# Performance work log

Hardware: AMD Instinct MI355X
Metric: run time of the kernel (lower is better)

Reference implementation:

```python
import jax, jax.numpy as jnp
import numpy as np

# NOTE: SoftAttn (not shown in source) is assumed to be a channel-wise softmax over the
# kernel_size**2 attention maps, as is standard in involution/dynamic-conv designs.

def conv2d(x, w, b=None, stride=1, pad=0, dil=1):
    y = jax.lax.conv_general_dilated(
        x, w, (stride, stride), [(pad, pad), (pad, pad)],
        rhs_dilation=(dil, dil), dimension_numbers=('NCHW', 'OIHW', 'NCHW'))
    return y if b is None else y + b[None, :, None, None]

def prelu(x, a):
    return jnp.where(x >= 0, x, a * x)

def pixel_shuffle(x, r):
    b, c, h, w = x.shape
    x = x.reshape(b, c // (r * r), r, r, h, w)
    x = x.transpose(0, 1, 4, 2, 5, 3)  # b, c', h, r, w, r
    return x.reshape(b, c // (r * r), h * r, w * r)

def aflb(x, aw, ab, fw):
    # Adaptive Fine-grained Local Block: per-position attention over k^2 taps,
    # broadcast across input channels, then contracted with the conv weight.
    k = 3
    C = x.shape[1]
    att = jax.nn.softmax(conv2d(x, aw, ab, pad=1), axis=1)  # [b, k*k, H, W]
    # unfold (channel-major, spatial-minor, matching torch F.unfold)
    p = jax.lax.conv_general_dilated_patches(
        x, (k, k), (1, 1), [(1, 1), (1, 1)],
        dimension_numbers=('NCHW', 'OIHW', 'NCHW'))  # [b, C*k*k, H, W]
    b_, _, H, W = p.shape
    p = p.reshape(b_, C, k * k, H, W)
    atx = p * att[:, None]  # broadcast attention over channels
    return jnp.einsum('bcphw,ocp->bohw', atx, fw.reshape(fw.shape[0], C, k * k))

def rmrs(x, wa, ba, wb, bb, wc, bc, awA, abA, fwA, awB, abB, fwB):
    o = jnp.concatenate([
        conv2d(x, wa, ba, pad=1),
        conv2d(x, wb, bb, pad=2, dil=2),
        conv2d(x, wc, bc, pad=3, dil=3)], axis=1)
    o = aflb(o, awA, abA, fwA)
    o = aflb(o, awB, abB, fwB)
    return jax.nn.relu(o + x)


def setup_inputs() -> dict:
    key = jax.random.key(0)
    ks = iter(jax.random.split(key, 64))
    def rn(shape, s=0.05):
        return jax.random.normal(next(ks), shape, jnp.float32) * s
    a = lambda: jnp.full((1,), 0.25, jnp.float32)
    d = dict(
        ms_up=rn((2, 4, 256, 256), 1.0),
        ms_org=rn((2, 4, 64, 64), 1.0),
        pan=rn((2, 1, 256, 256), 1.0),
        w_up4=rn((64, 4, 3, 3)), b_up4=jnp.zeros(64, jnp.float32), a_up4=a(),
        w_blk53=rn((30, 5, 3, 3)), b_blk53=jnp.zeros(30, jnp.float32), a_blk53=a(),
        w_blk43=rn((30, 4, 3, 3)), b_blk43=jnp.zeros(30, jnp.float32), a_blk43=a(),
        w1a=rn((20, 60, 3, 3)), b1a=jnp.zeros(20, jnp.float32),
        w1b=rn((20, 60, 3, 3)), b1b=jnp.zeros(20, jnp.float32),
        w1c=rn((20, 60, 3, 3)), b1c=jnp.zeros(20, jnp.float32),
        aw1=rn((9, 60, 3, 3)), ab1=jnp.zeros(9, jnp.float32), fw1=rn((60, 60, 3, 3)),
        aw2=rn((9, 60, 3, 3)), ab2=jnp.zeros(9, jnp.float32), fw2=rn((60, 60, 3, 3)),
        w_blk2=rn((30, 60, 3, 3)), b_blk2=jnp.zeros(30, jnp.float32), a_blk2=a(),
        w2a=rn((10, 30, 3, 3)), b2a=jnp.zeros(10, jnp.float32),
        w2b=rn((10, 30, 3, 3)), b2b=jnp.zeros(10, jnp.float32),
        w2c=rn((10, 30, 3, 3)), b2c=jnp.zeros(10, jnp.float32),
        aw3=rn((9, 30, 3, 3)), ab3=jnp.zeros(9, jnp.float32), fw3=rn((30, 30, 3, 3)),
        aw4=rn((9, 30, 3, 3)), ab4=jnp.zeros(9, jnp.float32), fw4=rn((30, 30, 3, 3)),
        w_c6=rn((4, 30, 3, 3)), b_c6=jnp.zeros(4, jnp.float32),
    )
    return d


def reference(ms_up, ms_org, pan,
              w_up4, b_up4, a_up4,
              w_blk53, b_blk53, a_blk53,
              w_blk43, b_blk43, a_blk43,
              w1a, b1a, w1b, b1b, w1c, b1c,
              aw1, ab1, fw1, aw2, ab2, fw2,
              w_blk2, b_blk2, a_blk2,
              w2a, b2a, w2b, b2b, w2c, b2c,
              aw3, ab3, fw3, aw4, ab4, fw4,
              w_c6, b_c6):
    ms_org_up = prelu(pixel_shuffle(conv2d(ms_org, w_up4, b_up4, pad=1), 4), a_up4)
    data1 = jnp.concatenate([ms_org_up, pan], axis=1)  # [b,5,H,W]
    pan_conv = prelu(conv2d(data1, w_blk53, b_blk53, pad=1), a_blk53)
    ms_up_conv = prelu(conv2d(ms_up, w_blk43, b_blk43, pad=1), a_blk43)
    out1 = jnp.concatenate([ms_up_conv, pan_conv], axis=1)  # [b,60,H,W]
    out2 = rmrs(out1, w1a, b1a, w1b, b1b, w1c, b1c, aw1, ab1, fw1, aw2, ab2, fw2)
    out3 = prelu(conv2d(out2, w_blk2, b_blk2, pad=1), a_blk2)  # [b,30,H,W]
    out3 = rmrs(out3, w2a, b2a, w2b, b2b, w2c, b2c, aw3, ab3, fw3, aw4, ab4, fw4)
    out8 = conv2d(out3, w_c6, b_c6, pad=1)
    return out8 + ms_up
```

## Files before the change

### kernel.cpp

```cpp
#include <hip/hip_runtime.h>

typedef __attribute__((ext_vector_type(8))) short short8;
typedef __attribute__((ext_vector_type(4))) float f32x4;
typedef __attribute__((ext_vector_type(4))) int i32x4;

#define HW 65536

__device__ __forceinline__ float bf2f(unsigned short u){
    union { unsigned int i; float f; } x; x.i = ((unsigned int)u) << 16; return x.f;
}
__device__ __forceinline__ unsigned short f2bf(float f){
    union { float f; unsigned int i; } x; x.f = f;
    unsigned int r = x.i + 0x7fffu + ((x.i >> 16) & 1u);
    return (unsigned short)(r >> 16);
}
__device__ __forceinline__ unsigned int pack2(float a, float b){
    return (unsigned int)f2bf(a) | ((unsigned int)f2bf(b) << 16);
}
__device__ __forceinline__ i32x4 addrelu4(i32x4 a, i32x4 b){
    i32x4 o;
#pragma unroll
    for (int k = 0; k < 4; ++k) {
        unsigned int ua = (unsigned int)a[k], ub = (unsigned int)b[k];
        float x0 = bf2f((unsigned short)(ua & 0xffff)) + bf2f((unsigned short)(ub & 0xffff));
        float x1 = bf2f((unsigned short)(ua >> 16))    + bf2f((unsigned short)(ub >> 16));
        o[k] = (int)(((unsigned int)f2bf(fmaxf(x0, 0.f))) |
                     ((unsigned int)f2bf(fmaxf(x1, 0.f)) << 16));
    }
    return o;
}

template<int KK, int PRELU>
__global__ __launch_bounds__(256, 4) void sconv_k(
    const unsigned short* __restrict__ in,
    const unsigned short* __restrict__ wfrag,
    const float* __restrict__ bias,
    const float* __restrict__ alphap,
    unsigned short* __restrict__ outb, int cpad, int coff)
{
    constexpr int CPIN = KK * 32, SGR = KK * 4, SGRP = SGR + 1, SPX = 66;
    constexpr int NSTGDW = 3 * SPX * SGRP * 4;
    constexpr int ODP = 20;
    constexpr int OUTOFF = NSTGDW;
    __shared__ __align__(16) unsigned int sm[NSTGDW + 64 * ODP];
    const int tid = threadIdx.x;
    const int lane = tid & 63, wv = tid >> 6;
    const int col = lane & 15, g = lane >> 4;
    const int bx = blockIdx.x;
    const int xcd = bx & 7, t = bx >> 3;
    const int y0 = xcd * 32 + (t & 31);
    const int x0 = ((t >> 5) & 3) * 64;
    const int b = blockIdx.z;
    const unsigned short* inb = in + (size_t)b * HW * CPIN;

#pragma unroll
    for (int rr = 0; rr < 3; ++rr) {
        const int yy = y0 + rr - 1;
        for (int u = tid; u < SPX * SGR; u += 256) {
            const int slot = u & (SGR - 1), px = u / SGR;
            const int xx = x0 - 1 + px;
            i32x4 v = {0,0,0,0};
            if ((unsigned)yy < 256u && (unsigned)xx < 256u)
                v = *(const i32x4*)(inb + (size_t)(yy * 256 + xx) * CPIN + slot * 8);
            *(i32x4*)&sm[((rr * SPX + px) * SGRP + slot) * 4] = v;
        }
    }
    if (tid < 64) sm[OUTOFF + tid * ODP + 15] = 0;
    __syncthreads();

    const short8* wp = (const short8*)wfrag;
    f32x4 acc[2][2];
#pragma unroll
    for (int mt = 0; mt < 2; ++mt)
#pragma unroll
        for (int c = 0; c < 2; ++c) acc[mt][c] = (f32x4){0.f,0.f,0.f,0.f};
#pragma unroll
    for (int tap = 0; tap < 9; ++tap) {
        const int dy = tap / 3 - 1, dx = tap % 3 - 1;
        const int rl = dy + 1;
        short8 af[2][KK];
#pragma unroll
        for (int mt = 0; mt < 2; ++mt)
#pragma unroll
            for (int kk = 0; kk < KK; ++kk)
                af[mt][kk] = wp[((tap * 2 + mt) * KK + kk) * 64 + lane];
        const int pl = 1 + wv * 16 + col + dx;
#pragma unroll
        for (int kk = 0; kk < KK; ++kk) {
            const int c2 = (KK == 2) ? kk : (tap & 1);
            short8 bf = *(const short8*)&sm[((rl * SPX + pl) * SGRP + kk * 4 + g) * 4];
#pragma unroll
            for (int mt = 0; mt < 2; ++mt)
                acc[mt][c2] = __builtin_amdgcn_mfma_f32_16x16x32_bf16(af[mt][kk], bf, acc[mt][c2], 0, 0, 0);
        }
    }
    const float al = PRELU ? __ldg(alphap) : 0.f;
    const int px = wv * 16 + col;
#pragma unroll
    for (int mt = 0; mt < 2; ++mt) {
        const f32x4 a = acc[mt][0] + acc[mt][1];
#pragma unroll
        for (int e = 0; e < 2; ++e) {
            const int rb = mt * 16 + g * 4 + e * 2;
            if (rb < 30) {
                float v0 = a[e * 2]     + __ldg(bias + rb);
                float v1 = a[e * 2 + 1] + ((rb + 1 < 30) ? __ldg(bias + rb + 1) : 0.f);
                if (PRELU) { v0 = v0 >= 0.f ? v0 : al * v0; v1 = v1 >= 0.f ? v1 : al * v1; }
                if (rb + 1 >= 30) v1 = 0.f;
                sm[OUTOFF + px * ODP + (rb >> 1)] = pack2(v0, v1);
            }
        }
    }
    __syncthreads();
    {
        const int slot = tid & 3, opx = tid >> 2;
        i32x4 v = *(i32x4*)&sm[OUTOFF + opx * ODP + slot * 4];
        const size_t go = ((size_t)b * HW + (size_t)y0 * 256 + x0 + opx) * cpad + coff + slot * 8;
        *(i32x4*)(outb + go) = v;
    }
}

template<int KK, int MR>
__global__ __launch_bounds__(256, 4) void trident_s(
    const unsigned short* __restrict__ in,
    const unsigned short* __restrict__ wf0, const unsigned short* __restrict__ wf1,
    const unsigned short* __restrict__ wf2,
    const float* __restrict__ b0, const float* __restrict__ b1, const float* __restrict__ b2,
    unsigned short* __restrict__ outb)
{
    constexpr int CPIN = KK * 32, CPAD = KK * 32;
    constexpr int SGR = KK * 4, SGRP = SGR + 1, SPX = 70;
    constexpr int MT_ = (KK == 2) ? 2 : 1;
    constexpr int CPP = KK * 4, ODP = (CPP + 1) * 4;
    constexpr int NSTGDW = 3 * SPX * SGRP * 4;
    constexpr int OUTOFF = NSTGDW;
    constexpr int NG1 = SPX * SGR;
    constexpr int NIT2 = (2 * NG1 + 255) / 256;
    __shared__ __align__(16) unsigned int sm[NSTGDW + 64 * ODP];
    const int tid = threadIdx.x;
    const int lane = tid & 63, wv = tid >> 6;
    const int col = lane & 15, g = lane >> 4;
    const int bx = blockIdx.x;
    const int xcd = bx & 7, t = bx >> 3;
    const int y0 = xcd * 32 + (t & 31);
    const int x0 = ((t >> 5) & 3) * 64;
    const int b = blockIdx.z;
    const unsigned short* inb = in + (size_t)b * HW * CPIN;

    auto stage_row = [&](int srow, int yy) {
        for (int u = tid; u < NG1; u += 256) {
            const int slot = u & (SGR - 1), px = u / SGR;
            const int xx = x0 - 3 + px;
            i32x4 v = {0,0,0,0};
            if ((unsigned)yy < 256u && (unsigned)xx < 256u)
                v = *(const i32x4*)(inb + (size_t)(yy * 256 + xx) * CPIN + slot * 8);
            *(i32x4*)&sm[((srow * SPX + px) * SGRP + slot) * 4] = v;
        }
    };
    i32x4 Rp[NIT2];
    auto issue_pair = [&](int d) {
#pragma unroll
        for (int it = 0; it < NIT2; ++it) {
            const int u = tid + it * 256;
            i32x4 v = {0,0,0,0};
            if (u < 2 * NG1) {
                const int r = (u >= NG1) ? 1 : 0;
                const int uu = u - r * NG1;
                const int slot = uu & (SGR - 1), px = uu / SGR;
                const int yy = y0 + (r ? d : -d);
                const int xx = x0 - 3 + px;
                if ((unsigned)yy < 256u && (unsigned)xx < 256u)
                    v = *(const i32x4*)(inb + (size_t)(yy * 256 + xx) * CPIN + slot * 8);
            }
            Rp[it] = v;
        }
    };
    auto write_pair = [&]() {
#pragma unroll
        for (int it = 0; it < NIT2; ++it) {
            const int u = tid + it * 256;
            if (u < 2 * NG1) {
                const int r = (u >= NG1) ? 1 : 0;
                const int uu = u - r * NG1;
                const int slot = uu & (SGR - 1), px = uu / SGR;
                *(i32x4*)&sm[(((1 + r) * SPX + px) * SGRP + slot) * 4] = Rp[it];
            }
        }
    };
    auto do_conv = [&](int d, const unsigned short* wfx, const float* bs, int which) {
        const short8* wp = (const short8*)wfx;
        f32x4 acc[MT_][2];
#pragma unroll
        for (int mt = 0; mt < MT_; ++mt)
#pragma unroll
            for (int c = 0; c < 2; ++c) acc[mt][c] = (f32x4){0.f,0.f,0.f,0.f};
#pragma unroll
        for (int tap = 0; tap < 9; ++tap) {
            const int dy = tap / 3 - 1, dx = tap % 3 - 1;
            const int rl = (dy == 0) ? 0 : (dy < 0 ? 1 : 2);
            short8 af[MT_][KK];
#pragma unroll
            for (int mt = 0; mt < MT_; ++mt)
#pragma unroll
                for (int kk = 0; kk < KK; ++kk)
                    af[mt][kk] = wp[((tap * MT_ + mt) * KK + kk) * 64 + lane];
            const int pl = 3 + wv * 16 + col + dx * d;
#pragma unroll
            for (int kk = 0; kk < KK; ++kk) {
                const int c2 = (KK == 2) ? kk : (tap & 1);
                short8 bf = *(const short8*)&sm[((rl * SPX + pl) * SGRP + kk * 4 + g) * 4];
#pragma unroll
                for (int mt = 0; mt < MT_; ++mt)
                    acc[mt][c2] = __builtin_amdgcn_mfma_f32_16x16x32_bf16(af[mt][kk], bf, acc[mt][c2], 0, 0, 0);
            }
        }
        const int px = wv * 16 + col;
#pragma unroll
        for (int mt = 0; mt < MT_; ++mt) {
            const f32x4 a = acc[mt][0] + acc[mt][1];
#pragma unroll
            for (int e = 0; e < 2; ++e) {
                const int rb = mt * 16 + g * 4 + e * 2;
                if (rb < MR) {
                    float v0 = a[e * 2]     + __ldg(bs + rb);
                    float v1 = a[e * 2 + 1] + ((rb + 1 < MR) ? __ldg(bs + rb + 1) : 0.f);
                    if (rb + 1 >= MR) v1 = 0.f;
                    sm[OUTOFF + px * ODP + ((which * MR + rb) >> 1)] = pack2(v0, v1);
                }
            }
        }
    };

    stage_row(0, y0); stage_row(1, y0 - 1); stage_row(2, y0 + 1);
    issue_pair(2);
    if (tid < 64) {
#pragma unroll
        for (int dwp = 3 * MR / 2; dwp < CPP * 4; ++dwp) sm[OUTOFF + tid * ODP + dwp] = 0;
    }
    __syncthreads();

    do_conv(1, wf0, b0, 0);
    __syncthreads();
    write_pair();
    issue_pair(3);
    __syncthreads();

    do_conv(2, wf1, b1, 1);
    __syncthreads();
    write_pair();
    __syncthreads();

    do_conv(3, wf2, b2, 2);
    __syncthreads();

    for (int u = tid; u < 64 * CPP; u += 256) {
        const int slot = u & (CPP - 1), opx = u / CPP;
        i32x4 v = *(i32x4*)&sm[OUTOFF + opx * ODP + slot * 4];
        const size_t go = ((size_t)b * HW + (size_t)y0 * 256 + x0 + opx) * CPAD + slot * 8;
        *(i32x4*)(outb + go) = v;
    }
}

template<int KK, int RPB, int RES>
__global__ __launch_bounds__(256, 4) void aflb_p(
    const unsigned short* __restrict__ in,
    const unsigned short* __restrict__ awf, const float* __restrict__ ab,
    const unsigned short* __restrict__ fwf,
    const unsigned short* __restrict__ res,
    unsigned short* __restrict__ outb)
{
    constexpr int CPIN = KK * 32, MTT = 2 * KK, CPAD = 16 * MTT;
    constexpr int SROWS = RPB + 2, SPX = 66, SGR = KK * 4, SGRP = SGR + 1;
    constexpr int CPP = CPAD / 8, ODP = (CPP + 1) * 4;
    constexpr int NSTGDW = SROWS * SPX * SGRP * 4;
    constexpr int ATOFF = NSTGDW;
    constexpr int NATT = RPB * 64 * 9;
    constexpr int OUTOFF = ATOFF + NATT;
    __shared__ __align__(16) unsigned int sm[OUTOFF + RPB * 64 * ODP];

    const int tid = threadIdx.x;
    const int lane = tid & 63, wv = tid >> 6;
    const int col = lane & 15, g = lane >> 4;
    const int bx = blockIdx.x;
    const int xcd = bx & 7, t = bx >> 3;
    const int y0 = (RPB == 1) ? (xcd * 32 + (t & 31)) : (xcd * 32 + (t & 15) * 2);
    const int xseg = (RPB == 1) ? ((t >> 5) & 3) : ((t >> 4) & 3);
    const int x0 = xseg * 64;
    const int b = blockIdx.z;
    const unsigned short* inb = in + (size_t)b * HW * CPIN;

    for (int u = tid; u < SROWS * SPX * SGR; u += 256) {
        const int slot = u & (SGR - 1);
        const int px = (u / SGR) % SPX;
        const int row = u / (SGR * SPX);
        const int yy = y0 + row - 1, xx = x0 - 1 + px;
        i32x4 v = {0,0,0,0};
        if ((unsigned)yy < 256u && (unsigned)xx < 256u)
            v = *(const i32x4*)(inb + (size_t)(yy * 256 + xx) * CPIN + slot * 8);
        *(i32x4*)&sm[((row * SPX + px) * SGRP + slot) * 4] = v;
    }
    __syncthreads();

    const short8* awp = (const short8*)awf;
    const short8* fwp = (const short8*)fwf;

    constexpr int NF1 = (RPB == 1) ? 1 : 2;
    const int arow = (RPB == 1) ? 0 : (wv >> 1);
    const int apx0 = (RPB == 1) ? (wv * 16) : ((wv & 1) * 32);
    f32x4 aacc[NF1][2];
#pragma unroll
    for (int nf = 0; nf < NF1; ++nf)
#pragma unroll
        for (int c = 0; c < 2; ++c) aacc[nf][c] = (f32x4){0.f,0.f,0.f,0.f};
#pragma unroll
    for (int tap = 0; tap < 9; ++tap) {
        const int dy = tap / 3 - 1, dx = tap % 3 - 1;
        const int rl = arow + dy + 1;
        short8 afa[KK];
#pragma unroll
        for (int kk = 0; kk < KK; ++kk)
            afa[kk] = awp[(tap * KK + kk) * 64 + lane];
#pragma unroll
        for (int nf = 0; nf < NF1; ++nf) {
            const int pl = 1 + apx0 + nf * 16 + col + dx;
#pragma unroll
            for (int kk = 0; kk < KK; ++kk) {
                const int c2 = (KK == 2) ? kk : (tap & 1);
                short8 bf = *(const short8*)&sm[((rl * SPX + pl) * SGRP + kk * 4 + g) * 4];
                aacc[nf][c2] = __builtin_amdgcn_mfma_f32_16x16x32_bf16(afa[kk], bf, aacc[nf][c2], 0, 0, 0);
            }
        }
    }
#pragma unroll
    for (int nf = 0; nf < NF1; ++nf) {
        const f32x4 aa = aacc[nf][0] + aacc[nf][1];
        float v[4];
        float m = -1e30f;
#pragma unroll
        for (int r = 0; r < 4; ++r) {
            const int row = g * 4 + r;
            v[r] = (row < 9) ? (aa[r] + __ldg(ab + row)) : -1e30f;
            m = fmaxf(m, v[r]);
        }
        m = fmaxf(m, __shfl_xor(m, 16));
        m = fmaxf(m, __shfl_xor(m, 32));
        float e[4]; float s = 0.f;
#pragma unroll
        for (int r = 0; r < 4; ++r) { e[r] = (g * 4 + r < 9) ? __expf(v[r] - m) : 0.f; s += e[r]; }
        s += __shfl_xor(s, 16);
        s += __shfl_xor(s, 32);
        const float inv = 1.f / s;
        const int px = apx0 + nf * 16 + col;
#pragma unroll
        for (int r = 0; r < 4; ++r) {
            const int row = g * 4 + r;
            if (row < 9) sm[ATOFF + (arow * 64 + px) * 9 + row] = __float_as_uint(e[r] * inv);
        }
    }
    __syncthreads();

    const int prow = (RPB == 1) ? 0 : (wv >> 1);
    const int mth  = (RPB == 1) ? (wv >> 1) : 0;
    const int nfh  = wv & 1;
    f32x4 acc[2][2];
#pragma unroll
    for (int mtl = 0; mtl < 2; ++mtl)
#pragma unroll
        for (int nf = 0; nf < 2; ++nf) acc[mtl][nf] = (f32x4){0.f,0.f,0.f,0.f};
#pragma unroll
    for (int tap = 0; tap < 9; ++tap) {
        const int dy = tap / 3 - 1, dx = tap % 3 - 1;
        const int rl = prow + dy + 1;
        float av[2];
#pragma unroll
        for (int nf = 0; nf < 2; ++nf)
            av[nf] = __uint_as_float(sm[ATOFF + (prow * 64 + nfh * 32 + nf * 16 + col) * 9 + tap]);
        short8 af[2][KK];
#pragma unroll
        for (int mtl = 0; mtl < 2; ++mtl)
#pragma unroll
            for (int kk = 0; kk < KK; ++kk)
                af[mtl][kk] = fwp[((tap * MTT + (RPB == 1 ? mth * 2 + mtl : mtl)) * KK + kk) * 64 + lane];
#pragma unroll
        for (int nf = 0; nf < 2; ++nf) {
            const int pl = 1 + nfh * 32 + nf * 16 + col + dx;
            f32x4 p[2];
            p[0] = (f32x4){0.f,0.f,0.f,0.f}; p[1] = (f32x4){0.f,0.f,0.f,0.f};
#pragma unroll
            for (int kk = 0; kk < KK; ++kk) {
                short8 bf = *(const short8*)&sm[((rl * SPX + pl) * SGRP + kk * 4 + g) * 4];
#pragma unroll
                for (int mtl = 0; mtl < 2; ++mtl)
                    p[mtl] = __builtin_amdgcn_mfma_f32_16x16x32_bf16(af[mtl][kk], bf, p[mtl], 0, 0, 0);
            }
#pragma unroll
            for (int mtl = 0; mtl < 2; ++mtl)
#pragma unroll
                for (int r = 0; r < 4; ++r)
                    acc[mtl][nf][r] = fmaf(av[nf], p[mtl][r], acc[mtl][nf][r]);
        }
    }
    __syncthreads();

#pragma unroll
    for (int mtl = 0; mtl < 2; ++mtl) {
        const int mt = (RPB == 1) ? (mth * 2 + mtl) : mtl;
#pragma unroll
        for (int nf = 0; nf < 2; ++nf) {
            const int px = nfh * 32 + nf * 16 + col;
            const int base = OUTOFF + ((RPB == 2 ? prow * 64 : 0) + px) * ODP;
            const int rp = mt * 8 + g * 2;
            unsigned long long w =
                (unsigned long long)pack2(acc[mtl][nf][0], acc[mtl][nf][1]) |
                ((unsigned long long)pack2(acc[mtl][nf][2], acc[mtl][nf][3]) << 32);
            *(unsigned long long*)&sm[base + rp] = w;
        }
    }
    __syncthreads();

    constexpr int NOUT = RPB * 64 * CPP;
    for (int u = tid; u < NOUT; u += 256) {
        const int slot = u & (CPP - 1);
        const int px = (u / CPP) & 63;
        const int r = (RPB == 2) ? (u / (CPP * 64)) : 0;
        i32x4 v = *(i32x4*)&sm[OUTOFF + ((r * 64 + px) * ODP) + slot * 4];
        const size_t go = ((size_t)b * HW + (size_t)(y0 + r) * 256 + x0 + px) * CPAD + slot * 8;
        if (RES) v = addrelu4(v, *(const i32x4*)(res + go));
        *(i32x4*)(outb + go) = v;
    }
}

__global__ __launch_bounds__(256, 4) void final_k(
    const unsigned short* __restrict__ in,
    const unsigned short* __restrict__ wfrag,
    const float* __restrict__ bias,
    const float* __restrict__ msup, float* __restrict__ outf)
{
    constexpr int CPIN = 32, NF = 2;
    const int lane = threadIdx.x & 63, wv = threadIdx.x >> 6;
    const int col = lane & 15, g = lane >> 4;
    const int bx = blockIdx.x;
    const int xcd = bx & 7, t = bx >> 3;
    const int y = xcd * 32 + (t & 31);
    const int xh = t >> 5;
    const int b = blockIdx.z;
    const int x0 = xh * 128 + wv * 32;

    const unsigned short* inb = in + (size_t)b * HW * CPIN;
    const short8 kz = {0,0,0,0,0,0,0,0};
    const short8* wp = (const short8*)wfrag;

    f32x4 acc[NF];
#pragma unroll
    for (int nf = 0; nf < NF; ++nf) acc[nf] = (f32x4){0.f,0.f,0.f,0.f};
#pragma unroll
    for (int tap = 0; tap < 9; ++tap) {
        const int dy = tap / 3 - 1, dx = tap % 3 - 1;
        const int yy = y + dy;
        const bool yok = (unsigned)yy < 256u;
        const short8 af = wp[tap * 64 + lane];
#pragma unroll
        for (int nf = 0; nf < NF; ++nf) {
            const int xx = x0 + nf * 16 + col + dx;
            const bool ok = yok && ((unsigned)xx < 256u);
            const int pix = ok ? (yy * 256 + xx) : 0;
            short8 bf = *(const short8*)(inb + (size_t)pix * CPIN + g * 8);
            if (!ok) bf = kz;
            acc[nf] = __builtin_amdgcn_mfma_f32_16x16x32_bf16(af, bf, acc[nf], 0, 0, 0);
        }
    }
#pragma unroll
    for (int nf = 0; nf < NF; ++nf) {
        const int pix = y * 256 + x0 + nf * 16 + col;
        if (g == 0) {
#pragma unroll
            for (int r = 0; r < 4; ++r) {
                const size_t oi = ((size_t)b * 4 + r) * HW + pix;
                outf[oi] = acc[nf][r] + __ldg(bias + r) + msup[oi];
            }
        }
    }
}

struct PrepDesc { const float* src; int cout, cin, kksh, mtsh, flags, dstoff, n; };
struct PrepArgs { PrepDesc d[18]; };

__global__ __launch_bounds__(256) void prep_k(PrepArgs pa, unsigned short* __restrict__ wb)
{
    const PrepDesc d = pa.d[blockIdx.y];
    const int e = blockIdx.x * 256 + threadIdx.x;
    if (e >= d.n) return;
    const int j = e & 7;
    const int lane = (e >> 3) & 63;
    const int i512 = e >> 9;
    const int kk = i512 & ((1 << d.kksh) - 1);
    const int mt = (i512 >> d.kksh) & ((1 << d.mtsh) - 1);
    const int tap = i512 >> (d.kksh + d.mtsh);
    const int rpos = mt * 16 + (lane & 15);
    const int kpos = kk * 32 + (lane >> 4) * 8 + j;
    int o = rpos, ic = kpos;
    bool ok = true;
    if (d.flags & 2) {
        if (rpos < 30) o = rpos;
        else if (rpos >= 32 && rpos < 62) o = rpos - 2;
        else ok = false;
    }
    if (d.flags & 1) {
        if (kpos < 30) ic = kpos;
        else if (kpos >= 32 && kpos < 62) ic = kpos - 2;
        else ok = false;
    }
    float v = 0.f;
    if (ok && o < d.cout && ic < d.cin) v = d.src[(o * d.cin + ic) * 9 + tap];
    wb[d.dstoff + e] = f2bf(v);
}

template<int CIN, int COUT, int OCB, int H, int W>
__launch_bounds__(256)
__global__ void upconv_k(const float* __restrict__ in, const float* __restrict__ wgt,
                         const float* __restrict__ bias, float* __restrict__ out)
{
    constexpr int HWp = H * W;
    constexpr int NOCB = COUT / OCB;
    const int tx = threadIdx.x;
    const int lx = tx & 63, ly = tx >> 6;
    const int gx = blockIdx.x * 64 + lx;
    const int gy = blockIdx.y * 4 + ly;
    const int b = blockIdx.z / NOCB;
    const int ocb = blockIdx.z % NOCB;
    const int pixp = gy * W + gx;
    const float* inb = in + (size_t)b * CIN * HWp;

    int off[9]; float mul[9];
#pragma unroll
    for (int dy = 0; dy < 3; ++dy)
#pragma unroll
        for (int dx = 0; dx < 3; ++dx) {
            int p = dy * 3 + dx;
            int yy = gy + dy - 1, xx = gx + dx - 1;
            bool okp = ((unsigned)yy < (unsigned)H) && ((unsigned)xx < (unsigned)W);
            off[p] = okp ? (yy * W + xx) : 0;
            mul[p] = okp ? 1.f : 0.f;
        }
    float acc[OCB];
#pragma unroll
    for (int o = 0; o < OCB; ++o) acc[o] = 0.f;
    const float* wbase = wgt + (size_t)(ocb * OCB) * CIN * 9;
#pragma unroll
    for (int ic = 0; ic < CIN; ++ic) {
        const float* ip = inb + (size_t)ic * HWp;
        float tv[9];
#pragma unroll
        for (int p = 0; p < 9; ++p) tv[p] = __ldg(ip + off[p]) * mul[p];
#pragma unroll
        for (int o = 0; o < OCB; ++o) {
            const float* wq = wbase + (size_t)(o * CIN + ic) * 9;
#pragma unroll
            for (int p = 0; p < 9; ++p) acc[o] = fmaf(tv[p], wq[p], acc[o]);
        }
    }
#pragma unroll
    for (int o = 0; o < OCB; ++o)
        out[((size_t)b * COUT + ocb * OCB + o) * HWp + pixp] = acc[o] + __ldg(bias + ocb * OCB + o);
}

__global__ __launch_bounds__(256) void build_inputs(
    const float* __restrict__ tup, const float* __restrict__ pan,
    const float* __restrict__ aup, const float* __restrict__ msup,
    unsigned short* __restrict__ data1, unsigned short* __restrict__ msb)
{
    const int i = blockIdx.x * 256 + threadIdx.x;
    const int b = i >> 16, pixp = i & 65535;
    const int y = pixp >> 8, x = pixp & 255;
    unsigned short o[32];
#pragma unroll
    for (int c = 0; c < 32; ++c) o[c] = 0;
    unsigned short* dst;
    if (blockIdx.y == 0) {
        const float a = __ldg(aup);
#pragma unroll
        for (int c = 0; c < 4; ++c) {
            const int ch = c * 16 + (y & 3) * 4 + (x & 3);
            float v = tup[(((size_t)b * 64 + ch) << 12) + ((y >> 2) << 6) + (x >> 2)];
            v = (v >= 0.f) ? v : a * v;
            o[c] = f2bf(v);
        }
        o[4] = f2bf(pan[((size_t)b << 16) + pixp]);
        dst = data1;
    } else {
#pragma unroll
        for (int c = 0; c < 4; ++c)
            o[c] = f2bf(msup[(((size_t)b * 4 + c) << 16) + pixp]);
        dst = msb;
    }
    short8* dp = (short8*)(dst + (size_t)i * 32);
#pragma unroll
    for (int q = 0; q < 4; ++q) {
        short8 s;
#pragma unroll
        for (int r = 0; r < 8; ++r) s[r] = (short)o[q * 8 + r];
        dp[q] = s;
    }
}

extern "C" void kernel_launch(void* const* d_in, const int* in_sizes, int n_in,
                              void* d_out, int out_size, void* d_ws, size_t ws_size,
                              hipStream_t stream) {
    const float* ms_up  = (const float*)d_in[0];
    const float* ms_org = (const float*)d_in[1];
    const float* pan    = (const float*)d_in[2];
    const float* w_up4  = (const float*)d_in[3];
    const float* b_up4  = (const float*)d_in[4];
    const float* a_up4  = (const float*)d_in[5];
    const float* w_blk53= (const float*)d_in[6];
    const float* b_blk53= (const float*)d_in[7];
    const float* a_blk53= (const float*)d_in[8];
    const float* w_blk43= (const float*)d_in[9];
    const float* b_blk43= (const float*)d_in[10];
    const float* a_blk43= (const float*)d_in[11];
    const float* w1a=(const float*)d_in[12]; const float* b1a=(const float*)d_in[13];
    const float* w1b=(const float*)d_in[14]; const float* b1b=(const float*)d_in[15];
    const float* w1c=(const float*)d_in[16]; const float* b1c=(const float*)d_in[17];
    const float* aw1=(const float*)d_in[18]; const float* ab1=(const float*)d_in[19];
    const float* fw1=(const float*)d_in[20];
    const float* aw2=(const float*)d_in[21]; const float* ab2=(const float*)d_in[22];
    const float* fw2=(const float*)d_in[23];
    const float* w_blk2=(const float*)d_in[24]; const float* b_blk2=(const float*)d_in[25]; const float* a_blk2=(const float*)d_in[26];
    const float* w2a=(const float*)d_in[27]; const float* b2a=(const float*)d_in[28];
    const float* w2b=(const float*)d_in[29]; const float* b2b=(const float*)d_in[30];
    const float* w2c=(const float*)d_in[31]; const float* b2c=(const float*)d_in[32];
    const float* aw3=(const float*)d_in[33]; const float* ab3=(const float*)d_in[34];
    const float* fw3=(const float*)d_in[35];
    const float* aw4=(const float*)d_in[36]; const float* ab4=(const float*)d_in[37];
    const float* fw4=(const float*)d_in[38];
    const float* w_c6=(const float*)d_in[39]; const float* b_c6=(const float*)d_in[40];

    float* out = (float*)d_out;
    char* ws = (char*)d_ws;

    const size_t BIG = (size_t)2 * HW * 64 * 2;
    const size_t HALF = BIG / 2;
    unsigned short* bufA = (unsigned short*)(ws);
    unsigned short* bufB = (unsigned short*)(ws + BIG);
    unsigned short* bufC = (unsigned short*)(ws + 2 * BIG);
    unsigned short* data1 = bufC;
    float*          t_up  = (float*)(ws + 2 * BIG + HALF);
    unsigned short* msb   = bufB;
    unsigned short* bufD = bufC;
    unsigned short* bufE = bufB;
    unsigned short* bufF = bufA;
    unsigned short* wb = (unsigned short*)(ws + 3 * BIG);

    if (ws_size < 3 * BIG + 1000000) return;

    PrepArgs pa;
    int off = 0, li = 0;
    auto add = [&](const float* s, int cout, int cin, int mtsh, int kksh, int flags) {
        const int n = 9 << (mtsh + kksh + 9);
        pa.d[li].src = s; pa.d[li].cout = cout; pa.d[li].cin = cin;
        pa.d[li].kksh = kksh; pa.d[li].mtsh = mtsh; pa.d[li].flags = flags;
        pa.d[li].dstoff = off; pa.d[li].n = n;
        int ret = off; off += n; ++li; return ret;
    };
    const int o_blk43 = add(w_blk43, 30, 4, 1, 0, 0);
    const int o_blk53 = add(w_blk53, 30, 5, 1, 0, 0);
    const int o_w1a   = add(w1a, 20, 60, 1, 1, 1);
    const int o_w1b   = add(w1b, 20, 60, 1, 1, 1);
    const int o_w1c   = add(w1c, 20, 60, 1, 1, 1);
    const int o_aw1   = add(aw1,  9, 60, 0, 1, 0);
    const int o_fw1   = add(fw1, 60, 60, 2, 1, 0);
    const int o_aw2   = add(aw2,  9, 60, 0, 1, 0);
    const int o_fw2   = add(fw2, 60, 60, 2, 1, 2);
    const int o_blk2  = add(w_blk2, 30, 60, 1, 1, 1);
    const int o_w2a   = add(w2a, 10, 30, 0, 0, 0);
    const int o_w2b   = add(w2b, 10, 30, 0, 0, 0);
    const int o_w2c   = add(w2c, 10, 30, 0, 0, 0);
    const int o_aw3   = add(aw3,  9, 30, 0, 0, 0);
    const int o_fw3   = add(fw3, 30, 30, 1, 0, 0);
    const int o_aw4   = add(aw4,  9, 30, 0, 0, 0);
    const int o_fw4   = add(fw4, 30, 30, 1, 0, 0);
    const int o_c6    = add(w_c6,  4, 30, 0, 0, 0);

    prep_k<<<dim3(144, 18), 256, 0, stream>>>(pa, wb);

    upconv_k<4, 64, 16, 64, 64><<<dim3(1, 16, 8), 256, 0, stream>>>(ms_org, w_up4, b_up4, t_up);
    build_inputs<<<dim3(512, 2), 256, 0, stream>>>(t_up, pan, a_up4, ms_up, data1, msb);

    const dim3 B256(256);
    const dim3 G1(1024, 1, 2);
    const dim3 GH(512, 1, 2);

    sconv_k<1,1><<<G1,B256,0,stream>>>(msb,   wb+o_blk43, b_blk43, a_blk43, bufA, 64, 0);
    sconv_k<1,1><<<G1,B256,0,stream>>>(data1, wb+o_blk53, b_blk53, a_blk53, bufA, 64, 32);

    trident_s<2,20><<<G1,B256,0,stream>>>(bufA, wb+o_w1a, wb+o_w1b, wb+o_w1c, b1a, b1b, b1c, bufB);
    aflb_p<2,1,0><<<G1,B256,0,stream>>>(bufB, wb+o_aw1, ab1, wb+o_fw1, nullptr, bufC);
    aflb_p<2,1,1><<<G1,B256,0,stream>>>(bufC, wb+o_aw2, ab2, wb+o_fw2, bufA,   bufB);

    sconv_k<2,1><<<G1,B256,0,stream>>>(bufB, wb+o_blk2, b_blk2, a_blk2, bufD, 32, 0);

    trident_s<1,10><<<G1,B256,0,stream>>>(bufD, wb+o_w2a, wb+o_w2b, wb+o_w2c, b2a, b2b, b2c, bufE);
    aflb_p<1,2,0><<<GH,B256,0,stream>>>(bufE, wb+o_aw3, ab3, wb+o_fw3, nullptr, bufF);
    aflb_p<1,2,1><<<GH,B256,0,stream>>>(bufF, wb+o_aw4, ab4, wb+o_fw4, bufD,   bufE);

    final_k<<<GH,B256,0,stream>>>(bufE, wb+o_c6, b_c6, ms_up, out);
}
```

Measured before the change: 205.8 us.

## Alias output staging onto input LDS buffer and raise occupancy launch bounds

Removes the separate output-staging region from shared memory in sconv, trident and aflb kernels by reusing the input staging area after a barrier. This shrinks the LDS footprint per block so more blocks can be resident, and the launch bounds are raised to request that higher occupancy. In trident, per-branch conv results are now held in registers until all three convs finish, which adds register pressure. The tighter launch bounds also risk register spills.

```diff
diff --git a/kernel.cpp b/kernel.cpp
--- a/kernel.cpp
+++ b/kernel.cpp
@@ -31,7 +31,7 @@
 }
 
 template<int KK, int PRELU>
-__global__ __launch_bounds__(256, 4) void sconv_k(
+__global__ __launch_bounds__(256, (KK == 2 ? 5 : 8)) void sconv_k(
     const unsigned short* __restrict__ in,
     const unsigned short* __restrict__ wfrag,
     const float* __restrict__ bias,
@@ -41,8 +41,7 @@
     constexpr int CPIN = KK * 32, SGR = KK * 4, SGRP = SGR + 1, SPX = 66;
     constexpr int NSTGDW = 3 * SPX * SGRP * 4;
     constexpr int ODP = 20;
-    constexpr int OUTOFF = NSTGDW;
-    __shared__ __align__(16) unsigned int sm[NSTGDW + 64 * ODP];
+    __shared__ __align__(16) unsigned int sm[NSTGDW];
     const int tid = threadIdx.x;
     const int lane = tid & 63, wv = tid >> 6;
     const int col = lane & 15, g = lane >> 4;
@@ -65,7 +64,6 @@
             *(i32x4*)&sm[((rr * SPX + px) * SGRP + slot) * 4] = v;
         }
     }
-    if (tid < 64) sm[OUTOFF + tid * ODP + 15] = 0;
     __syncthreads();
 
     const short8* wp = (const short8*)wfrag;
@@ -94,6 +92,8 @@
                 acc[mt][c2] = __builtin_amdgcn_mfma_f32_16x16x32_bf16(af[mt][kk], bf, acc[mt][c2], 0, 0, 0);
         }
     }
+    __syncthreads();
+
     const float al = PRELU ? __ldg(alphap) : 0.f;
     const int px = wv * 16 + col;
 #pragma unroll
@@ -102,26 +102,23 @@
 #pragma unroll
         for (int e = 0; e < 2; ++e) {
             const int rb = mt * 16 + g * 4 + e * 2;
-            if (rb < 30) {
-                float v0 = a[e * 2]     + __ldg(bias + rb);
-                float v1 = a[e * 2 + 1] + ((rb + 1 < 30) ? __ldg(bias + rb + 1) : 0.f);
-                if (PRELU) { v0 = v0 >= 0.f ? v0 : al * v0; v1 = v1 >= 0.f ? v1 : al * v1; }
-                if (rb + 1 >= 30) v1 = 0.f;
-                sm[OUTOFF + px * ODP + (rb >> 1)] = pack2(v0, v1);
-            }
+            float v0 = (rb < 30)     ? a[e * 2]     + __ldg(bias + rb)     : 0.f;
+            float v1 = (rb + 1 < 30) ? a[e * 2 + 1] + __ldg(bias + rb + 1) : 0.f;
+            if (PRELU) { v0 = v0 >= 0.f ? v0 : al * v0; v1 = v1 >= 0.f ? v1 : al * v1; }
+            sm[px * ODP + (rb >> 1)] = pack2(v0, v1);
         }
     }
     __syncthreads();
     {
         const int slot = tid & 3, opx = tid >> 2;
-        i32x4 v = *(i32x4*)&sm[OUTOFF + opx * ODP + slot * 4];
+        i32x4 v = *(i32x4*)&sm[opx * ODP + slot * 4];
         const size_t go = ((size_t)b * HW + (size_t)y0 * 256 + x0 + opx) * cpad + coff + slot * 8;
         *(i32x4*)(outb + go) = v;
     }
 }
 
 template<int KK, int MR>
-__global__ __launch_bounds__(256, 4) void trident_s(
+__global__ __launch_bounds__(256, (KK == 2 ? 5 : 8)) void trident_s(
     const unsigned short* __restrict__ in,
     const unsigned short* __restrict__ wf0, const unsigned short* __restrict__ wf1,
     const unsigned short* __restrict__ wf2,
@@ -133,10 +130,9 @@
     constexpr int MT_ = (KK == 2) ? 2 : 1;
     constexpr int CPP = KK * 4, ODP = (CPP + 1) * 4;
     constexpr int NSTGDW = 3 * SPX * SGRP * 4;
-    constexpr int OUTOFF = NSTGDW;
     constexpr int NG1 = SPX * SGR;
     constexpr int NIT2 = (2 * NG1 + 255) / 256;
-    __shared__ __align__(16) unsigned int sm[NSTGDW + 64 * ODP];
+    __shared__ __align__(16) unsigned int sm[NSTGDW];
     const int tid = threadIdx.x;
     const int lane = tid & 63, wv = tid >> 6;
     const int col = lane & 15, g = lane >> 4;
@@ -187,7 +183,9 @@
             }
         }
     };
-    auto do_conv = [&](int d, const unsigned short* wfx, const float* bs, int which) {
+
+    f32x4 resv[3][MT_];
+    auto do_conv = [&](int d, const unsigned short* wfx, int which) {
         const short8* wp = (const short8*)wfx;
         f32x4 acc[MT_][2];
 #pragma unroll
@@ -214,55 +212,62 @@
                     acc[mt][c2] = __builtin_amdgcn_mfma_f32_16x16x32_bf16(af[mt][kk], bf, acc[mt][c2], 0, 0, 0);
             }
         }
-        const int px = wv * 16 + col;
-#pragma unroll
-        for (int mt = 0; mt < MT_; ++mt) {
-            const f32x4 a = acc[mt][0] + acc[mt][1];
-#pragma unroll
-            for (int e = 0; e < 2; ++e) {
-                const int rb = mt * 16 + g * 4 + e * 2;
-                if (rb < MR) {
-                    float v0 = a[e * 2]     + __ldg(bs + rb);
-                    float v1 = a[e * 2 + 1] + ((rb + 1 < MR) ? __ldg(bs + rb + 1) : 0.f);
-                    if (rb + 1 >= MR) v1 = 0.f;
-                    sm[OUTOFF + px * ODP + ((which * MR + rb) >> 1)] = pack2(v0, v1);
-                }
-            }
-        }
+#pragma unroll
+        for (int mt = 0; mt < MT_; ++mt)
+            resv[which][mt] = acc[mt][0] + acc[mt][1];
     };
 
     stage_row(0, y0); stage_row(1, y0 - 1); stage_row(2, y0 + 1);
     issue_pair(2);
-    if (tid < 64) {
-#pragma unroll
-        for (int dwp = 3 * MR / 2; dwp < CPP * 4; ++dwp) sm[OUTOFF + tid * ODP + dwp] = 0;
-    }
-    __syncthreads();
-
-    do_conv(1, wf0, b0, 0);
+    __syncthreads();
+
+    do_conv(1, wf0, 0);
     __syncthreads();
     write_pair();
     issue_pair(3);
     __syncthreads();
 
-    do_conv(2, wf1, b1, 1);
+    do_conv(2, wf1, 1);
     __syncthreads();
     write_pair();
     __syncthreads();
 
-    do_conv(3, wf2, b2, 2);
+    do_conv(3, wf2, 2);
+    __syncthreads();
+
+    {
+        const float* bss[3] = {b0, b1, b2};
+        const int px = wv * 16 + col;
+#pragma unroll
+        for (int which = 0; which < 3; ++which)
+#pragma unroll
+            for (int mt = 0; mt < MT_; ++mt)
+#pragma unroll
+                for (int e = 0; e < 2; ++e) {
+                    const int rb = mt * 16 + g * 4 + e * 2;
+                    if (rb < MR) {
+                        float v0 = resv[which][mt][e * 2] + __ldg(bss[which] + rb);
+                        float v1 = (rb + 1 < MR) ? resv[which][mt][e * 2 + 1] + __ldg(bss[which] + rb + 1) : 0.f;
+                        sm[px * ODP + ((which * MR + rb) >> 1)] = pack2(v0, v1);
+                    }
+                }
+        if (tid < 64) {
+#pragma unroll
+            for (int dwp = 3 * MR / 2; dwp < CPP * 4; ++dwp) sm[tid * ODP + dwp] = 0;
+        }
+    }
     __syncthreads();
 
     for (int u = tid; u < 64 * CPP; u += 256) {
         const int slot = u & (CPP - 1), opx = u / CPP;
-        i32x4 v = *(i32x4*)&sm[OUTOFF + opx * ODP + slot * 4];
+        i32x4 v = *(i32x4*)&sm[opx * ODP + slot * 4];
         const size_t go = ((size_t)b * HW + (size_t)y0 * 256 + x0 + opx) * CPAD + slot * 8;
         *(i32x4*)(outb + go) = v;
     }
 }
 
 template<int KK, int RPB, int RES>
-__global__ __launch_bounds__(256, 4) void aflb_p(
+__global__ __launch_bounds__(256, (KK == 2 ? 5 : 6)) void aflb_p(
     const unsigned short* __restrict__ in,
     const unsigned short* __restrict__ awf, const float* __restrict__ ab,
     const unsigned short* __restrict__ fwf,
@@ -275,8 +280,7 @@
     constexpr int NSTGDW = SROWS * SPX * SGRP * 4;
     constexpr int ATOFF = NSTGDW;
     constexpr int NATT = RPB * 64 * 9;
-    constexpr int OUTOFF = ATOFF + NATT;
-    __shared__ __align__(16) unsigned int sm[OUTOFF + RPB * 64 * ODP];
+    __shared__ __align__(16) unsigned int sm[ATOFF + NATT];
 
     const int tid = threadIdx.x;
     const int lane = tid & 63, wv = tid >> 6;
@@ -408,7 +412,7 @@
 #pragma unroll
         for (int nf = 0; nf < 2; ++nf) {
             const int px = nfh * 32 + nf * 16 + col;
-            const int base = OUTOFF + ((RPB == 2 ? prow * 64 : 0) + px) * ODP;
+            const int base = ((RPB == 2 ? prow * 64 : 0) + px) * ODP;
             const int rp = mt * 8 + g * 2;
             unsigned long long w =
                 (unsigned long long)pack2(acc[mtl][nf][0], acc[mtl][nf][1]) |
@@ -423,14 +427,14 @@
         const int slot = u & (CPP - 1);
         const int px = (u / CPP) & 63;
         const int r = (RPB == 2) ? (u / (CPP * 64)) : 0;
-        i32x4 v = *(i32x4*)&sm[OUTOFF + ((r * 64 + px) * ODP) + slot * 4];
+        i32x4 v = *(i32x4*)&sm[((r * 64 + px) * ODP) + slot * 4];
         const size_t go = ((size_t)b * HW + (size_t)(y0 + r) * 256 + x0 + px) * CPAD + slot * 8;
         if (RES) v = addrelu4(v, *(const i32x4*)(res + go));
         *(i32x4*)(outb + go) = v;
     }
 }
 
-__global__ __launch_bounds__(256, 4) void final_k(
+__global__ __launch_bounds__(256, 8) void final_k(
     const unsigned short* __restrict__ in,
     const unsigned short* __restrict__ wfrag,
     const float* __restrict__ bias,
```

Result: slower. 216.1 us (+5.0%).

## Run trident dilation branches in parallel warps with swizzled 7-row LDS tile

Applied to the files above, without the earlier changes.

Replaces the sequential three-dilation trident kernel with one where 6 wavefronts (2 per dilation) compute the three dilated convolutions concurrently over a 32-pixel-wide tile. The whole 7-row halo is staged once, with an XOR swizzle in place of padded LDS strides, so the per-dilation row-pair reloads and intermediate barriers go away. Block size grows to 384 and the grid doubles. In exchange, horizontal halo overhead per block is higher (38 staged columns for 32 outputs) and each block loads more rows.

```diff
diff --git a/kernel.cpp b/kernel.cpp
--- a/kernel.cpp
+++ b/kernel.cpp
@@ -121,7 +121,7 @@
 }
 
 template<int KK, int MR>
-__global__ __launch_bounds__(256, 4) void trident_s(
+__global__ __launch_bounds__(384, 6) void trident_v(
     const unsigned short* __restrict__ in,
     const unsigned short* __restrict__ wf0, const unsigned short* __restrict__ wf1,
     const unsigned short* __restrict__ wf2,
@@ -129,92 +129,69 @@
     unsigned short* __restrict__ outb)
 {
     constexpr int CPIN = KK * 32, CPAD = KK * 32;
-    constexpr int SGR = KK * 4, SGRP = SGR + 1, SPX = 70;
+    constexpr int SGR = KK * 4, SWM = SGR - 1, SPX = 38, SROWS = 7;
     constexpr int MT_ = (KK == 2) ? 2 : 1;
-    constexpr int CPP = KK * 4, ODP = (CPP + 1) * 4;
-    constexpr int NSTGDW = 3 * SPX * SGRP * 4;
-    constexpr int OUTOFF = NSTGDW;
-    constexpr int NG1 = SPX * SGR;
-    constexpr int NIT2 = (2 * NG1 + 255) / 256;
-    __shared__ __align__(16) unsigned int sm[NSTGDW + 64 * ODP];
+    constexpr int CPP = KK * 4;
+    constexpr int NSTG = SROWS * SPX * SGR;
+    __shared__ __align__(16) unsigned int sm[NSTG * 4];
+
     const int tid = threadIdx.x;
     const int lane = tid & 63, wv = tid >> 6;
     const int col = lane & 15, g = lane >> 4;
     const int bx = blockIdx.x;
     const int xcd = bx & 7, t = bx >> 3;
     const int y0 = xcd * 32 + (t & 31);
-    const int x0 = ((t >> 5) & 3) * 64;
+    const int x0 = ((t >> 5) & 7) * 32;
     const int b = blockIdx.z;
     const unsigned short* inb = in + (size_t)b * HW * CPIN;
 
-    auto stage_row = [&](int srow, int yy) {
-        for (int u = tid; u < NG1; u += 256) {
-            const int slot = u & (SGR - 1), px = u / SGR;
-            const int xx = x0 - 3 + px;
-            i32x4 v = {0,0,0,0};
-            if ((unsigned)yy < 256u && (unsigned)xx < 256u)
-                v = *(const i32x4*)(inb + (size_t)(yy * 256 + xx) * CPIN + slot * 8);
-            *(i32x4*)&sm[((srow * SPX + px) * SGRP + slot) * 4] = v;
-        }
-    };
-    i32x4 Rp[NIT2];
-    auto issue_pair = [&](int d) {
-#pragma unroll
-        for (int it = 0; it < NIT2; ++it) {
-            const int u = tid + it * 256;
-            i32x4 v = {0,0,0,0};
-            if (u < 2 * NG1) {
-                const int r = (u >= NG1) ? 1 : 0;
-                const int uu = u - r * NG1;
-                const int slot = uu & (SGR - 1), px = uu / SGR;
-                const int yy = y0 + (r ? d : -d);
-                const int xx = x0 - 3 + px;
-                if ((unsigned)yy < 256u && (unsigned)xx < 256u)
-                    v = *(const i32x4*)(inb + (size_t)(yy * 256 + xx) * CPIN + slot * 8);
-            }
-            Rp[it] = v;
-        }
-    };
-    auto write_pair = [&]() {
-#pragma unroll
-        for (int it = 0; it < NIT2; ++it) {
-            const int u = tid + it * 256;
-            if (u < 2 * NG1) {
-                const int r = (u >= NG1) ? 1 : 0;
-                const int uu = u - r * NG1;
-                const int slot = uu & (SGR - 1), px = uu / SGR;
-                *(i32x4*)&sm[(((1 + r) * SPX + px) * SGRP + slot) * 4] = Rp[it];
-            }
-        }
-    };
-    auto do_conv = [&](int d, const unsigned short* wfx, const float* bs, int which) {
-        const short8* wp = (const short8*)wfx;
-        f32x4 acc[MT_][2];
+    for (int u = tid; u < NSTG; u += 384) {
+        const int slot = u & SWM;
+        const int px = (u / SGR) % SPX;
+        const int row = u / (SGR * SPX);
+        const int yy = y0 + row - 3, xx = x0 - 3 + px;
+        i32x4 v = {0,0,0,0};
+        if ((unsigned)yy < 256u && (unsigned)xx < 256u)
+            v = *(const i32x4*)(inb + (size_t)(yy * 256 + xx) * CPIN + slot * 8);
+        *(i32x4*)&sm[((row * SPX + px) * SGR + (slot ^ (px & SWM))) * 4] = v;
+    }
+    __syncthreads();
+
+    const int dil = wv >> 1, d = dil + 1, xh = wv & 1;
+    const unsigned short* wfx = (dil == 0) ? wf0 : ((dil == 1) ? wf1 : wf2);
+    const float* bs = (dil == 0) ? b0 : ((dil == 1) ? b1 : b2);
+    const short8* wp = (const short8*)wfx;
+
+    f32x4 acc[MT_][2];
+#pragma unroll
+    for (int mt = 0; mt < MT_; ++mt)
+#pragma unroll
+        for (int c = 0; c < 2; ++c) acc[mt][c] = (f32x4){0.f,0.f,0.f,0.f};
+
+#pragma unroll
+    for (int tap = 0; tap < 9; ++tap) {
+        const int dy = tap / 3 - 1, dx = tap % 3 - 1;
+        const int rl = 3 + dy * d;
+        short8 af[MT_][KK];
 #pragma unroll
         for (int mt = 0; mt < MT_; ++mt)
 #pragma unroll
-            for (int c = 0; c < 2; ++c) acc[mt][c] = (f32x4){0.f,0.f,0.f,0.f};
-#pragma unroll
-        for (int tap = 0; tap < 9; ++tap) {
-            const int dy = tap / 3 - 1, dx = tap % 3 - 1;
-            const int rl = (dy == 0) ? 0 : (dy < 0 ? 1 : 2);
-            short8 af[MT_][KK];
+            for (int kk = 0; kk < KK; ++kk)
+                af[mt][kk] = wp[((tap * MT_ + mt) * KK + kk) * 64 + lane];
+        const int pl = 3 + xh * 16 + col + dx * d;
+#pragma unroll
+        for (int kk = 0; kk < KK; ++kk) {
+            const int c2 = (KK == 2) ? kk : (tap & 1);
+            short8 bf = *(const short8*)&sm[((rl * SPX + pl) * SGR + ((kk * 4 + g) ^ (pl & SWM))) * 4];
 #pragma unroll
             for (int mt = 0; mt < MT_; ++mt)
-#pragma unroll
-                for (int kk = 0; kk < KK; ++kk)
-                    af[mt][kk] = wp[((tap * MT_ + mt) * KK + kk) * 64 + lane];
-            const int pl = 3 + wv * 16 + col + dx * d;
-#pragma unroll
-            for (int kk = 0; kk < KK; ++kk) {
-                const int c2 = (KK == 2) ? kk : (tap & 1);
-                short8 bf = *(const short8*)&sm[((rl * SPX + pl) * SGRP + kk * 4 + g) * 4];
-#pragma unroll
-                for (int mt = 0; mt < MT_; ++mt)
-                    acc[mt][c2] = __builtin_amdgcn_mfma_f32_16x16x32_bf16(af[mt][kk], bf, acc[mt][c2], 0, 0, 0);
-            }
-        }
-        const int px = wv * 16 + col;
+                acc[mt][c2] = __builtin_amdgcn_mfma_f32_16x16x32_bf16(af[mt][kk], bf, acc[mt][c2], 0, 0, 0);
+        }
+    }
+    __syncthreads();
+
+    {
+        const int px = xh * 16 + col;
 #pragma unroll
         for (int mt = 0; mt < MT_; ++mt) {
             const f32x4 a = acc[mt][0] + acc[mt][1];
@@ -222,40 +199,24 @@
             for (int e = 0; e < 2; ++e) {
                 const int rb = mt * 16 + g * 4 + e * 2;
                 if (rb < MR) {
-                    float v0 = a[e * 2]     + __ldg(bs + rb);
-                    float v1 = a[e * 2 + 1] + ((rb + 1 < MR) ? __ldg(bs + rb + 1) : 0.f);
-                    if (rb + 1 >= MR) v1 = 0.f;
-                    sm[OUTOFF + px * ODP + ((which * MR + rb) >> 1)] = pack2(v0, v1);
+                    float v0 = a[e * 2] + __ldg(bs + rb);
+                    float v1 = (rb + 1 < MR) ? a[e * 2 + 1] + __ldg(bs + rb + 1) : 0.f;
+                    const int dwp = (dil * MR + rb) >> 1;
+                    sm[px * CPP * 4 + (((dwp >> 2) ^ (px & SWM)) << 2) + (dwp & 3)] = pack2(v0, v1);
                 }
             }
         }
-    };
-
-    stage_row(0, y0); stage_row(1, y0 - 1); stage_row(2, y0 + 1);
-    issue_pair(2);
-    if (tid < 64) {
-#pragma unroll
-        for (int dwp = 3 * MR / 2; dwp < CPP * 4; ++dwp) sm[OUTOFF + tid * ODP + dwp] = 0;
-    }
-    __syncthreads();
-
-    do_conv(1, wf0, b0, 0);
-    __syncthreads();
-    write_pair();
-    issue_pair(3);
-    __syncthreads();
-
-    do_conv(2, wf1, b1, 1);
-    __syncthreads();
-    write_pair();
-    __syncthreads();
-
-    do_conv(3, wf2, b2, 2);
-    __syncthreads();
-
-    for (int u = tid; u < 64 * CPP; u += 256) {
+        constexpr int NPAD = CPP * 4 - 3 * MR / 2;
+        if (tid < 32 * NPAD) {
+            const int px = tid / NPAD, dwp = 3 * MR / 2 + tid % NPAD;
+            sm[px * CPP * 4 + (((dwp >> 2) ^ (px & SWM)) << 2) + (dwp & 3)] = 0;
+        }
+    }
+    __syncthreads();
+
+    for (int u = tid; u < 32 * CPP; u += 384) {
         const int slot = u & (CPP - 1), opx = u / CPP;
-        i32x4 v = *(i32x4*)&sm[OUTOFF + opx * ODP + slot * 4];
+        i32x4 v = *(i32x4*)&sm[opx * CPP * 4 + ((slot ^ (opx & SWM)) << 2)];
         const size_t go = ((size_t)b * HW + (size_t)y0 * 256 + x0 + opx) * CPAD + slot * 8;
         *(i32x4*)(outb + go) = v;
     }
@@ -686,20 +647,21 @@
     upconv_k<4, 64, 16, 64, 64><<<dim3(1, 16, 8), 256, 0, stream>>>(ms_org, w_up4, b_up4, t_up);
     build_inputs<<<dim3(512, 2), 256, 0, stream>>>(t_up, pan, a_up4, ms_up, data1, msb);
 
-    const dim3 B256(256);
+    const dim3 B256(256), B384(384);
     const dim3 G1(1024, 1, 2);
+    const dim3 GV(2048, 1, 2);
     const dim3 GH(512, 1, 2);
 
     sconv_k<1,1><<<G1,B256,0,stream>>>(msb,   wb+o_blk43, b_blk43, a_blk43, bufA, 64, 0);
     sconv_k<1,1><<<G1,B256,0,stream>>>(data1, wb+o_blk53, b_blk53, a_blk53, bufA, 64, 32);
 
-    trident_s<2,20><<<G1,B256,0,stream>>>(bufA, wb+o_w1a, wb+o_w1b, wb+o_w1c, b1a, b1b, b1c, bufB);
+    trident_v<2,20><<<GV,B384,0,stream>>>(bufA, wb+o_w1a, wb+o_w1b, wb+o_w1c, b1a, b1b, b1c, bufB);
     aflb_p<2,1,0><<<G1,B256,0,stream>>>(bufB, wb+o_aw1, ab1, wb+o_fw1, nullptr, bufC);
     aflb_p<2,1,1><<<G1,B256,0,stream>>>(bufC, wb+o_aw2, ab2, wb+o_fw2, bufA,   bufB);
 
     sconv_k<2,1><<<G1,B256,0,stream>>>(bufB, wb+o_blk2, b_blk2, a_blk2, bufD, 32, 0);
 
-    trident_s<1,10><<<G1,B256,0,stream>>>(bufD, wb+o_w2a, wb+o_w2b, wb+o_w2c, b2a, b2b, b2c, bufE);
+    trident_v<1,10><<<GV,B384,0,stream>>>(bufD, wb+o_w2a, wb+o_w2b, wb+o_w2c, b2a, b2b, b2c, bufE);
     aflb_p<1,2,0><<<GH,B256,0,stream>>>(bufE, wb+o_aw3, ab3, wb+o_fw3, nullptr, bufF);
     aflb_p<1,2,1><<<GH,B256,0,stream>>>(bufF, wb+o_aw4, ab4, wb+o_fw4, bufD,   bufE);
 
```

After: 209.5 us. Within noise of the previous version (+1.8%).
